# Optimization experiments

Hardware: AMD Instinct MI355X
Metric: run time of the kernel (lower is better)

The kernel has to match this reference:

```python
import jax, jax.numpy as jnp
import numpy as np

# Detect.__init__ defaults from the source
TOP_K = 5000
CONF_THRESH = 0.01
NMS_THRESH = 0.3
VAR0, VAR1 = 0.1, 0.2   # variance = [0.1, 0.2]
NUM_CLASSES = 2

B = 16
IMAGE = 1280
FMAPS = [320, 160, 80, 40, 20, 10]          # image / steps [4,8,16,32,64,128]
MIN_SIZES = [16, 32, 64, 128, 256, 512]
AR = 1.5                                     # aspect_ratios = [[1.5]] * 6


def make_priors():
    """Vectorized PriorBox.forward: 1 prior per location (max_sizes=[], single AR)."""
    chunks = []
    for f, ms in zip(FMAPS, MIN_SIZES):
        c = (np.arange(f, dtype=np.float32) + 0.5) / f
        cy, cx = np.meshgrid(c, c, indexing='ij')
        s = ms / float(IMAGE)
        w = np.full_like(cx, s / np.sqrt(AR))   # s_k / sqrt(ar)
        h = np.full_like(cx, s * np.sqrt(AR))   # s_k * sqrt(ar)
        chunks.append(np.stack([cx, cy, w, h], -1).reshape(-1, 4))
    pr = np.concatenate(chunks, 0).clip(0.0, 1.0)   # clip=True
    return jnp.asarray(pr, jnp.float32)             # [136500, 4]


def setup_inputs() -> dict:
    key = jax.random.key(0)
    k1, k2 = jax.random.split(key)
    P = sum(f * f for f in FMAPS)   # 136500
    loc_data = 0.5 * jax.random.normal(k1, (B, P, 4), jnp.float32)
    conf_data = jax.random.uniform(k2, (B * P, NUM_CLASSES), jnp.float32)  # post-softmax probs
    prior_data = make_priors()
    return {"loc_data": loc_data, "conf_data": conf_data, "prior_data": prior_data}


def _decode(loc, priors):
    # SSD box decode with variances [0.1, 0.2]; loc, priors: [P,4]
    cxcy = priors[:, :2] + loc[:, :2] * VAR0 * priors[:, 2:]
    wh = priors[:, 2:] * jnp.exp(loc[:, 2:] * VAR1)
    xy1 = cxcy - wh * 0.5
    xy2 = xy1 + wh
    return jnp.concatenate([xy1, xy2], axis=-1)   # [P,4] x1y1x2y2


def _greedy_keep(boxes, valid):
    # Greedy NMS over score-sorted candidates. boxes [K,4], valid [K] bool.
    # Indices/keep decisions are discrete -> computed on stop_gradient'd boxes.
    b = jax.lax.stop_gradient(boxes)
    x1, y1, x2, y2 = b[:, 0], b[:, 1], b[:, 2], b[:, 3]
    area = (x2 - x1) * (y2 - y1)
    idxs = jnp.arange(b.shape[0])

    def body(keep, i):
        iw = jnp.maximum(jnp.minimum(x2, x2[i]) - jnp.maximum(x1, x1[i]), 0.0)
        ih = jnp.maximum(jnp.minimum(y2, y2[i]) - jnp.maximum(y1, y1[i]), 0.0)
        inter = iw * ih
        iou = inter / (area + area[i] - inter)
        suppress = keep[i] & (iou > NMS_THRESH) & (idxs > i)
        return keep & ~suppress, None

    keep, _ = jax.lax.scan(body, valid, idxs)
    return keep


def _detect_one(loc_i, conf_cl, priors):
    # loc_i [P,4]; conf_cl [P] = class-1 scores; returns [TOP_K, 5] (score, x1,y1,x2,y2)
    boxes = _decode(loc_i, priors)
    masked = jnp.where(conf_cl > CONF_THRESH, conf_cl, -1.0)   # c_mask gating
    order = jnp.argsort(-jax.lax.stop_gradient(masked))[:TOP_K]  # scores.sort, top_k cap
    s = masked[order]
    b = boxes[order]
    valid = s > CONF_THRESH
    keep = _greedy_keep(b, valid)
    # scatter kept (score, box) rows, in descending-score order, into dense output
    rank = jnp.cumsum(keep) - 1
    row = jnp.where(keep, rank, TOP_K)            # dropped rows -> scratch slot
    vals = jnp.concatenate([s[:, None], b], axis=1)
    vals = jnp.where(keep[:, None], vals, 0.0)
    out = jnp.zeros((TOP_K + 1, 5), jnp.float32).at[row].set(vals)
    return out[:TOP_K]


def reference(loc_data, conf_data, prior_data):
    num = loc_data.shape[0]
    P = prior_data.shape[0]
    conf_preds = conf_data.reshape(num, P, NUM_CLASSES).transpose(0, 2, 1)  # [B,2,P]
    cls1 = jax.vmap(_detect_one, in_axes=(0, 0, None))(loc_data, conf_preds[:, 1, :], prior_data)
    bg = jnp.zeros_like(cls1)                     # background class row stays zero
    output = jnp.stack([bg, cls1], axis=1)        # [B, 2, TOP_K, 5]
    # NOTE: the original's final `flt[(rank < top_k)...].fill_(0)` fills a boolean-indexed
    # COPY in torch, so it is a no-op on `output`; we faithfully return output unchanged.
    return output
```

## Files before the change

kernel.cpp:

```cpp
#include <hip/hip_runtime.h>
#include <math.h>

#pragma clang fp contract(off)

#define PNUM 136500
#define HPNUM 68250
#define BNUM 16
#define TOPK 5000
#define CAP 8192
#define NB2 1024
#define B2BASE 0xBC00u
#define NWORDS 79
#define NW32 158
#define GSTRIDE 32
#define CAPE 65536
#define ELDS 10240
#define NXB 128
#define NWC 8
#define NXB2 1024
#define BSTRIDE 5120
#define EBUF 3072
#define SLOTS 4

#define OFF_SC    ((size_t)0)
#define OFF_BOX4  (OFF_SC + 320000)
#define OFF_HIST  (OFF_BOX4 + 1280000)
#define OFF_GBCUR (OFF_HIST + 65536)
#define OFF_ECNT  (OFF_GBCUR + 1048576)
#define OFF_BCNT  (OFF_ECNT + 2048)
#define OFF_BCUR  (OFF_BCNT + 65536)
#define OFF_ZEND  (OFF_BCUR + 65536)
#define OFF_CUT   (OFF_ZEND)
#define OFF_SBASE (OFF_CUT + 64)
#define OFF_KEYS  (OFF_SBASE + 65536)
#define OFF_EDGE  (OFF_KEYS + 1048576)
#define OFF_GRP   (OFF_EDGE + 4194304)
#define OFF_BOFS  (OFF_GRP)
#define OFF_SIDX  (OFF_GRP + 16384)
#define OFF_SBOX  (OFF_SIDX + 327680)

__device__ __forceinline__ unsigned f2ord(float f) {
    unsigned u = __float_as_uint(f);
    return (u & 0x80000000u) ? ~u : (u | 0x80000000u);
}
__device__ __forceinline__ float ord2f(unsigned o) {
    unsigned u = (o & 0x80000000u) ? (o ^ 0x80000000u) : ~o;
    return __uint_as_float(u);
}
__device__ __forceinline__ int bucketOf(float x) {
    int b = (int)((x + 0.6f) * 71.111115f);
    return (b < 0) ? 0 : ((b > 127) ? 127 : b);
}
__device__ __forceinline__ int rkeyOf(float x1, float x2) {
    int b = bucketOf(x1);
    int wc = bucketOf(x2) - b;
    if (wc > NWC - 1) wc = NWC - 1;
    if (wc < 0) wc = 0;
    return b * NWC + wc;
}

__global__ void __launch_bounds__(512) k_hist(const float* __restrict__ conf,
                                              unsigned* __restrict__ hist) {
    __shared__ unsigned lh[NB2];
    int img = blockIdx.y;
    for (int i = threadIdx.x; i < NB2; i += 512) lh[i] = 0;
    __syncthreads();
    const float4* src = (const float4*)(conf + (size_t)img * PNUM * 2);
    int stride = gridDim.x * 512;
    for (int q = blockIdx.x * 512 + threadIdx.x; q < HPNUM; q += stride) {
        float4 v = src[q];
        if (v.y > 0.01f) atomicAdd(&lh[(f2ord(v.y) >> 16) - B2BASE], 1u);
        if (v.w > 0.01f) atomicAdd(&lh[(f2ord(v.w) >> 16) - B2BASE], 1u);
    }
    __syncthreads();
    unsigned* h = hist + (size_t)img * NB2;
    for (int i = threadIdx.x; i < NB2; i += 512) {
        unsigned c = lh[i];
        if (c) atomicAdd(&h[i], c);
    }
}

__global__ void __launch_bounds__(256) k_cutoff2(const unsigned* __restrict__ hist,
                                                 unsigned* __restrict__ cut,
                                                 unsigned* __restrict__ sbase) {
    __shared__ unsigned csum[256], suf[256];
    int img = blockIdx.x;
    int t = threadIdx.x;
    const unsigned* h = hist + (size_t)img * NB2;
    unsigned h0 = h[t * 4], h1 = h[t * 4 + 1], h2 = h[t * 4 + 2], h3 = h[t * 4 + 3];
    csum[t] = h0 + h1 + h2 + h3;
    __syncthreads();
    if (t == 0) {
        unsigned a = 0;
        for (int g = 255; g >= 0; --g) { unsigned c = csum[g]; suf[g] = a; a += c; }
        unsigned acc = 0, before = 0;
        int c = -1;
        for (int cc = 255; cc >= 0; --cc) {
            if (acc + csum[cc] >= (unsigned)TOPK) { c = cc; before = acc; break; }
            acc += csum[cc];
        }
        unsigned cutb = B2BASE;
        if (c >= 0) {
            unsigned s2 = before;
            cutb = B2BASE + (unsigned)c * 4u;
            for (int b = c * 4 + 3; b >= c * 4; --b) {
                s2 += h[b];
                if (s2 >= (unsigned)TOPK) { cutb = B2BASE + (unsigned)b; break; }
            }
        }
        cut[img] = cutb;
    }
    __syncthreads();
    unsigned a = suf[t];
    unsigned* sb = sbase + (size_t)img * NB2 + t * 4;
    sb[3] = a;
    sb[2] = a + h3;
    sb[1] = a + h3 + h2;
    sb[0] = a + h3 + h2 + h1;
}

__global__ void __launch_bounds__(256) k_gather2(
        const float* __restrict__ conf, const unsigned* __restrict__ cut,
        const unsigned* __restrict__ sbase, unsigned* __restrict__ gbcur,
        unsigned long long* __restrict__ keys) {
    int q = blockIdx.x * 256 + threadIdx.x;
    int img = blockIdx.y;
    if (q >= HPNUM) return;
    unsigned cutb = cut[img];
    float4 v = ((const float4*)(conf + (size_t)img * PNUM * 2))[q];
    const unsigned* sb = sbase + (size_t)img * NB2;
    unsigned* gc = gbcur + (size_t)img * NB2 * 16;
    unsigned long long* kp = keys + (size_t)img * CAP;
    #pragma unroll
    for (int e = 0; e < 2; ++e) {
        float s = e ? v.w : v.y;
        if (s > 0.01f) {
            unsigned o = f2ord(s);
            if ((o >> 16) >= cutb) {
                unsigned wb = (o >> 16) - B2BASE;
                unsigned pos = sb[wb] + atomicAdd(&gc[wb * 16], 1u);
                if (pos < (unsigned)CAP)
                    kp[pos] = ((unsigned long long)o << 32)
                              | (unsigned)(~(unsigned)(2 * q + e));
            }
        }
    }
}

__global__ void __launch_bounds__(256) k_ssortdec(
        const unsigned long long* __restrict__ keys,
        const unsigned* __restrict__ hist, const unsigned* __restrict__ cut,
        const unsigned* __restrict__ sbase,
        const float* __restrict__ loc, const float* __restrict__ pri,
        float* __restrict__ SC, float4* __restrict__ BOX4,
        unsigned* __restrict__ bcnt) {
    __shared__ unsigned long long sk[1024];
    __shared__ unsigned lhist[NXB2];
    int img = blockIdx.y;
    int b = blockIdx.x;
    if (B2BASE + (unsigned)b < cut[img]) return;
    unsigned cnt = hist[(size_t)img * NB2 + b];
    if (cnt == 0) return;
    unsigned base = sbase[(size_t)img * NB2 + b];
    if (base >= (unsigned)TOPK) return;
    const unsigned long long* kp = keys + (size_t)img * CAP + base;
    int tid = threadIdx.x;
    for (int i = tid; i < NXB2; i += 256) lhist[i] = 0;
    unsigned scnt = cnt > 1024 ? 1024u : cnt;
    if (scnt >= 2) {
        unsigned np2 = 2;
        while (np2 < scnt) np2 <<= 1;
        for (unsigned i = tid; i < np2; i += 256) sk[i] = (i < scnt) ? kp[i] : 0ull;
        __syncthreads();
        for (unsigned k = 2; k <= np2; k <<= 1) {
            for (unsigned j = k >> 1; j > 0; j >>= 1) {
                for (unsigned t = tid; t < (np2 >> 1); t += 256) {
                    unsigned i = ((t & ~(j - 1)) << 1) | (t & (j - 1));
                    unsigned p = i | j;
                    bool desc = ((i & k) == 0);
                    unsigned long long a = sk[i], bb = sk[p];
                    bool sw = desc ? (a < bb) : (a > bb);
                    if (sw) { sk[i] = bb; sk[p] = a; }
                }
                __syncthreads();
            }
        }
    } else {
        if (tid == 0 && scnt == 1) sk[0] = kp[0];
        __syncthreads();
    }
    size_t ibase = (size_t)img * TOPK;
    for (unsigned i = tid; i < cnt; i += 256) {
        unsigned r = base + i;
        if (r >= (unsigned)TOPK) continue;
        unsigned long long key = (i < scnt) ? sk[i] : kp[i];
        float s, x1, y1, x2, y2;
        if (key != 0ull) {
            unsigned ordv = (unsigned)(key >> 32);
            s = ord2f(ordv);
            unsigned p = ~(unsigned)(key & 0xFFFFFFFFull);
            const float* lp = loc + ((size_t)img * PNUM + p) * 4;
            const float* pp = pri + (size_t)p * 4;
            float lx = lp[0], ly = lp[1], lw = lp[2], lh = lp[3];
            float px = pp[0], py = pp[1], pw = pp[2], ph = pp[3];
            float cx = px + (lx * 0.1f) * pw;
            float cy = py + (ly * 0.1f) * ph;
            float w = pw * expf(lw * 0.2f);
            float h = ph * expf(lh * 0.2f);
            x1 = cx - w * 0.5f;
            y1 = cy - h * 0.5f;
            x2 = x1 + w;
            y2 = y1 + h;
        } else {
            s = -1.0f; x1 = 0.f; y1 = 0.f; x2 = 0.f; y2 = 0.f;
        }
        SC[ibase + r] = s;
        BOX4[ibase + r] = make_float4(x1, y1, x2, y2);
        atomicAdd(&lhist[rkeyOf(x1, x2)], 1u);
    }
    __syncthreads();
    for (int i = tid; i < NXB2; i += 256) {
        unsigned c = lhist[i];
        if (c) atomicAdd(&bcnt[img * NXB2 + i], c);
    }
}

__global__ void __launch_bounds__(256) k_bscat(
        const unsigned* __restrict__ bcnt, unsigned* __restrict__ bcur,
        const float4* __restrict__ BOX4,
        unsigned* __restrict__ bofs, unsigned* __restrict__ sidx,
        float4* __restrict__ sbox) {
    __shared__ unsigned bpre[NXB2 + 1], tsum[256];
    int img = blockIdx.y;
    int tid = threadIdx.x;
    const unsigned* bc = bcnt + img * NXB2;
    unsigned l0 = bc[tid * 4], l1 = bc[tid * 4 + 1],
             l2 = bc[tid * 4 + 2], l3 = bc[tid * 4 + 3];
    tsum[tid] = l0 + l1 + l2 + l3;
    __syncthreads();
    if (tid == 0) {
        unsigned a = 0;
        for (int t = 0; t < 256; ++t) { unsigned c = tsum[t]; tsum[t] = a; a += c; }
        bpre[NXB2] = a;
    }
    __syncthreads();
    unsigned a = tsum[tid];
    bpre[tid * 4] = a;
    bpre[tid * 4 + 1] = a + l0;
    bpre[tid * 4 + 2] = a + l0 + l1;
    bpre[tid * 4 + 3] = a + l0 + l1 + l2;
    __syncthreads();
    if (blockIdx.x == 0) {
        if (tid < NXB) bofs[img * 130 + tid] = bpre[tid * NWC];
        if (tid == 0) bofs[img * 130 + NXB] = bpre[NXB2];
    }
    int r = blockIdx.x * 256 + tid;
    if (r < TOPK) {
        float4 b = BOX4[(size_t)img * TOPK + r];
        int bk = rkeyOf(b.x, b.z);
        unsigned s = bpre[bk] + atomicAdd(&bcur[img * NXB2 + bk], 1u);
        int base = img * BSTRIDE;
        sidx[base + s] = (unsigned)r;
        sbox[base + s] = b;
    }
}

__global__ void __launch_bounds__(256) k_pair4(
        const unsigned* __restrict__ bofs, const unsigned* __restrict__ sidx,
        const float4* __restrict__ sbox,
        unsigned* __restrict__ ecnt, unsigned* __restrict__ edges) {
    __shared__ unsigned ebuf[EBUF];
    __shared__ unsigned ecl, ebase;
    int img = blockIdx.y;
    int wid = threadIdx.x >> 6;
    int lane = threadIdx.x & 63;
    int sb0 = (blockIdx.x * 4 + wid) * SLOTS;
    if (threadIdx.x == 0) ecl = 0;
    __syncthreads();
    unsigned* ec = ecnt + (size_t)img * GSTRIDE;
    unsigned* eg = edges + (size_t)img * CAPE;
    if (sb0 < TOPK) {
        int base = img * BSTRIDE;
        float x1k[SLOTS], x2k[SLOTS], y1k[SLOTS], y2k[SLOTS], ark[SLOTS];
        unsigned rk[SLOTS];
        bool act[SLOTS];
        #pragma unroll
        for (int k = 0; k < SLOTS; ++k) {
            act[k] = (sb0 + k) < TOPK;
            int s = act[k] ? (sb0 + k) : sb0;
            float4 bk = sbox[base + s];
            x1k[k] = bk.x; y1k[k] = bk.y; x2k[k] = bk.z; y2k[k] = bk.w;
            ark[k] = (bk.z - bk.x) * (bk.w - bk.y);
            rk[k] = sidx[base + s];
        }
        int b1 = bucketOf(x1k[0]);
        int b2m = bucketOf(x2k[0]);
        #pragma unroll
        for (int k = 1; k < SLOTS; ++k)
            if (act[k]) { int b = bucketOf(x2k[k]); if (b > b2m) b2m = b; }
        const unsigned* bo = bofs + img * 130;
        unsigned s0 = bo[b1], s1 = bo[b2m + 1];
        if (s0 < s1) {
            unsigned nit = (s1 - s0 + 63) >> 6;
            unsigned c0 = s0 + (unsigned)lane;
            if (c0 > s1 - 1) c0 = s1 - 1;
            float4 cb = sbox[base + c0];
            unsigned cr = sidx[base + c0];
            for (unsigned it = 0; it < nit; ++it) {
                float4 nb = cb; unsigned nr = cr;
                if (it + 1 < nit) {
                    unsigned cn = s0 + (it + 1) * 64 + (unsigned)lane;
                    if (cn > s1 - 1) cn = s1 - 1;
                    nb = sbox[base + cn];
                    nr = sidx[base + cn];
                }
                bool in = (s0 + it * 64 + (unsigned)lane) < s1;
                float bar = (cb.z - cb.x) * (cb.w - cb.y);
                #pragma unroll
                for (int k = 0; k < SLOTS; ++k) {
                    bool hit = false;
                    unsigned edge = 0;
                    if (in && act[k] && cb.x >= x1k[k]
                        && !(cb.x == x1k[k] && cr <= rk[k])) {
                        float dx = fminf(x2k[k], cb.z) - fmaxf(x1k[k], cb.x);
                        if (dx > 0.0f) {
                            float dy = fminf(y2k[k], cb.w) - fmaxf(y1k[k], cb.y);
                            if (dy > 0.0f) {
                                float inter = dx * dy;
                                float iou = inter / (bar + ark[k] - inter);
                                if (iou > 0.3f) {
                                    unsigned su = (rk[k] < cr) ? rk[k] : cr;
                                    unsigned vi = (rk[k] < cr) ? cr : rk[k];
                                    edge = (vi << 13) | su;
                                    hit = true;
                                }
                            }
                        }
                    }
                    unsigned long long bal = __ballot(hit);
                    if (bal) {
                        int n = __popcll(bal);
                        unsigned wb = 0;
                        if (lane == 0) wb = atomicAdd(&ecl, (unsigned)n);
                        wb = __shfl(wb, 0, 64);
                        if (hit) {
                            unsigned long long lt =
                                (lane == 0) ? 0ull : ((1ull << lane) - 1ull);
                            unsigned p = wb + (unsigned)__popcll(bal & lt);
                            if (p < (unsigned)EBUF) ebuf[p] = edge;
                            else {
                                unsigned gp = atomicAdd(ec, 1u);
                                if (gp < (unsigned)CAPE) eg[gp] = edge;
                            }
                        }
                    }
                }
                cb = nb; cr = nr;
            }
        }
    }
    __syncthreads();
    unsigned n = min(ecl, (unsigned)EBUF);
    if (threadIdx.x == 0 && n) ebase = atomicAdd(ec, n);
    __syncthreads();
    for (unsigned i = threadIdx.x; i < n; i += 256) {
        unsigned p = ebase + i;
        if (p < (unsigned)CAPE) eg[p] = ebuf[i];
    }
}

__global__ void __launch_bounds__(256) k_nms3(
        const float* __restrict__ SC, const float4* __restrict__ BOX4,
        const unsigned* __restrict__ ecnt, const unsigned* __restrict__ edges,
        float* __restrict__ out) {
    __shared__ unsigned lgrp[ELDS];
    __shared__ unsigned undL[160], keptL[160], blockL[160];
    __shared__ unsigned pfx[80];
    __shared__ int chg[2];
    int img = blockIdx.x;
    int tid = threadIdx.x;
    int l = tid & 63;
    int wid = tid >> 6;
    size_t ib = (size_t)img * TOPK;
    const float* sc = SC + ib;

    float* oimg = out + (size_t)img * 2 * TOPK * 5;
    uint4* oz = (uint4*)oimg;
    uint4 z4 = make_uint4(0u, 0u, 0u, 0u);
    for (int i = tid; i < 12500; i += 256) oz[i] = z4;

    if (tid < 160) { keptL[tid] = 0u; blockL[tid] = 0u; }
    if (tid < 2) chg[tid] = 0;
    for (int w = wid; w < NWORDS; w += 4) {
        int row = w * 64 + l;
        bool valid = (row < TOPK) && (sc[row] > 0.01f);
        unsigned long long b = __ballot(valid);
        if (l == 0) {
            undL[2 * w]     = (unsigned)b;
            undL[2 * w + 1] = (unsigned)(b >> 32);
        }
    }
    unsigned E = min(ecnt[(size_t)img * GSTRIDE], (unsigned)CAPE);
    const unsigned* eimg = edges + (size_t)img * CAPE;
    bool inl = (E <= (unsigned)ELDS);
    if (inl) for (unsigned e = tid; e < E; e += 256) lgrp[e] = eimg[e];
    __syncthreads();

    for (int round = 0; round < 256; ++round) {
        int par = round & 1;
        for (unsigned e = tid; e < E; e += 256) {
            unsigned ed = inl ? lgrp[e] : eimg[e];
            unsigned s = ed & 8191u;
            unsigned v = ed >> 13;
            unsigned sw = s >> 5, sb = s & 31u;
            unsigned vw = v >> 5, vb = 1u << (v & 31u);
            if ((keptL[sw] >> sb) & 1u) {
                if (undL[vw] & vb) {
                    unsigned old = atomicAnd(&undL[vw], ~vb);
                    if (old & vb) chg[par] = 1;
                }
            } else if ((undL[sw] >> sb) & 1u) {
                if (!(blockL[vw] & vb)) atomicOr(&blockL[vw], vb);
            }
        }
        __syncthreads();
        if (tid < NW32) {
            unsigned nk = undL[tid] & ~blockL[tid];
            if (nk) {
                keptL[tid] |= nk;
                undL[tid] &= ~nk;
                chg[par] = 1;
            }
            blockL[tid] = 0u;
        }
        if (tid == 0) chg[par ^ 1] = 0;
        __syncthreads();
        if (!chg[par]) break;
    }

    if (tid == 0) {
        unsigned acc = 0;
        for (int w = 0; w < NWORDS; ++w) {
            pfx[w] = acc;
            acc += (unsigned)(__popc(keptL[2 * w]) + __popc(keptL[2 * w + 1]));
        }
    }
    __syncthreads();
    const float4* bx = BOX4 + ib;
    float* op = oimg + (size_t)TOPK * 5;
    for (int w = wid; w < NWORDS; w += 4) {
        unsigned long long kw =
            ((unsigned long long)keptL[2 * w + 1] << 32) | keptL[2 * w];
        if (!kw) continue;
        int row = w * 64 + l;
        if ((kw >> l) & 1ull) {
            int rank = (int)pfx[w] + (int)__popcll(kw & ((1ull << l) - 1ull));
            float4 b = bx[row];
            float* r = op + (size_t)rank * 5;
            r[0] = sc[row]; r[1] = b.x; r[2] = b.y; r[3] = b.z; r[4] = b.w;
        }
    }
}

extern "C" void kernel_launch(void* const* d_in, const int* in_sizes, int n_in,
                              void* d_out, int out_size, void* d_ws, size_t ws_size,
                              hipStream_t stream) {
    (void)in_sizes; (void)n_in; (void)ws_size; (void)out_size;
    const float* loc  = (const float*)d_in[0];
    const float* conf = (const float*)d_in[1];
    const float* pri  = (const float*)d_in[2];
    float* out = (float*)d_out;
    char* ws = (char*)d_ws;

    float* SC   = (float*)(ws + OFF_SC);
    float4* BOX4 = (float4*)(ws + OFF_BOX4);
    unsigned* hist = (unsigned*)(ws + OFF_HIST);
    unsigned* cut  = (unsigned*)(ws + OFF_CUT);
    unsigned* sbase = (unsigned*)(ws + OFF_SBASE);
    unsigned* gbcur = (unsigned*)(ws + OFF_GBCUR);
    unsigned long long* keys = (unsigned long long*)(ws + OFF_KEYS);
    unsigned* ecnt = (unsigned*)(ws + OFF_ECNT);
    unsigned* bcnt = (unsigned*)(ws + OFF_BCNT);
    unsigned* bcur = (unsigned*)(ws + OFF_BCUR);
    unsigned* edges = (unsigned*)(ws + OFF_EDGE);
    unsigned* bofs = (unsigned*)(ws + OFF_BOFS);
    unsigned* sidx = (unsigned*)(ws + OFF_SIDX);
    float4* sbox = (float4*)(ws + OFF_SBOX);

    hipMemsetAsync(ws + OFF_HIST, 0, OFF_ZEND - OFF_HIST, stream);

    dim3 gh1(16, BNUM);
    k_hist<<<gh1, 512, 0, stream>>>(conf, hist);
    k_cutoff2<<<BNUM, 256, 0, stream>>>(hist, cut, sbase);
    dim3 gh2((HPNUM + 255) / 256, BNUM);
    k_gather2<<<gh2, 256, 0, stream>>>(conf, cut, sbase, gbcur, keys);
    dim3 gs(NB2, BNUM);
    k_ssortdec<<<gs, 256, 0, stream>>>(keys, hist, cut, sbase,
                                       loc, pri, SC, BOX4, bcnt);
    dim3 gb((TOPK + 255) / 256, BNUM);
    k_bscat<<<gb, 256, 0, stream>>>(bcnt, bcur, BOX4, bofs, sidx, sbox);
    dim3 pg((TOPK + 4 * SLOTS - 1) / (4 * SLOTS), BNUM);
    k_pair4<<<pg, 256, 0, stream>>>(bofs, sidx, sbox, ecnt, edges);
    k_nms3<<<BNUM, 256, 0, stream>>>(SC, BOX4, ecnt, edges, out);
}
```

Measured before the change: 232.9 us.

## Refine score histogram to 4096 bins and sort only non-empty buckets via worklist

The score histogram moves from 1024 to 4096 finer bins (shift 14 instead of 16), so each bucket that must be bitonic-sorted holds fewer keys. The cutoff kernel now emits a compact worklist of non-empty buckets at or above the cutoff, and the sort/decode kernel runs a persistent grid of 1024 blocks that walks that list instead of launching NB2×16 blocks that mostly exit early. Shared-memory sort indices are padded to reduce bank conflicts and the gather counter stride shrinks. The tradeoffs are a global atomic per worklist entry, a larger histogram and workspace, and serial per-bucket loops inside each persistent block.

```diff
diff --git a/kernel.cpp b/kernel.cpp
--- a/kernel.cpp
+++ b/kernel.cpp
@@ -8,8 +8,9 @@
 #define BNUM 16
 #define TOPK 5000
 #define CAP 8192
-#define NB2 1024
-#define B2BASE 0xBC00u
+#define NB4 4096
+#define WBASE 0x2F000u
+#define GCS 4
 #define NWORDS 79
 #define NW32 158
 #define GSTRIDE 32
@@ -21,18 +22,21 @@
 #define BSTRIDE 5120
 #define EBUF 3072
 #define SLOTS 4
+#define SKI(i) ((i) + ((i) >> 4))
 
 #define OFF_SC    ((size_t)0)
 #define OFF_BOX4  (OFF_SC + 320000)
 #define OFF_HIST  (OFF_BOX4 + 1280000)
-#define OFF_GBCUR (OFF_HIST + 65536)
+#define OFF_GBCUR (OFF_HIST + 262144)
 #define OFF_ECNT  (OFF_GBCUR + 1048576)
 #define OFF_BCNT  (OFF_ECNT + 2048)
 #define OFF_BCUR  (OFF_BCNT + 65536)
-#define OFF_ZEND  (OFF_BCUR + 65536)
+#define OFF_WCNT  (OFF_BCUR + 65536)
+#define OFF_ZEND  (OFF_WCNT + 64)
 #define OFF_CUT   (OFF_ZEND)
 #define OFF_SBASE (OFF_CUT + 64)
-#define OFF_KEYS  (OFF_SBASE + 65536)
+#define OFF_WL    (OFF_SBASE + 262144)
+#define OFF_KEYS  (OFF_WL + 262144)
 #define OFF_EDGE  (OFF_KEYS + 1048576)
 #define OFF_GRP   (OFF_EDGE + 4194304)
 #define OFF_BOFS  (OFF_GRP)
@@ -61,20 +65,20 @@
 
 __global__ void __launch_bounds__(512) k_hist(const float* __restrict__ conf,
                                               unsigned* __restrict__ hist) {
-    __shared__ unsigned lh[NB2];
+    __shared__ unsigned lh[NB4];
     int img = blockIdx.y;
-    for (int i = threadIdx.x; i < NB2; i += 512) lh[i] = 0;
+    for (int i = threadIdx.x; i < NB4; i += 512) lh[i] = 0;
     __syncthreads();
     const float4* src = (const float4*)(conf + (size_t)img * PNUM * 2);
     int stride = gridDim.x * 512;
     for (int q = blockIdx.x * 512 + threadIdx.x; q < HPNUM; q += stride) {
         float4 v = src[q];
-        if (v.y > 0.01f) atomicAdd(&lh[(f2ord(v.y) >> 16) - B2BASE], 1u);
-        if (v.w > 0.01f) atomicAdd(&lh[(f2ord(v.w) >> 16) - B2BASE], 1u);
-    }
-    __syncthreads();
-    unsigned* h = hist + (size_t)img * NB2;
-    for (int i = threadIdx.x; i < NB2; i += 512) {
+        if (v.y > 0.01f) atomicAdd(&lh[(f2ord(v.y) >> 14) - WBASE], 1u);
+        if (v.w > 0.01f) atomicAdd(&lh[(f2ord(v.w) >> 14) - WBASE], 1u);
+    }
+    __syncthreads();
+    unsigned* h = hist + (size_t)img * NB4;
+    for (int i = threadIdx.x; i < NB4; i += 512) {
         unsigned c = lh[i];
         if (c) atomicAdd(&h[i], c);
     }
@@ -82,13 +86,18 @@
 
 __global__ void __launch_bounds__(256) k_cutoff2(const unsigned* __restrict__ hist,
                                                  unsigned* __restrict__ cut,
-                                                 unsigned* __restrict__ sbase) {
-    __shared__ unsigned csum[256], suf[256];
+                                                 unsigned* __restrict__ sbase,
+                                                 unsigned* __restrict__ wl,
+                                                 unsigned* __restrict__ wcnt) {
+    __shared__ unsigned csum[256], suf[256], scut;
     int img = blockIdx.x;
     int t = threadIdx.x;
-    const unsigned* h = hist + (size_t)img * NB2;
-    unsigned h0 = h[t * 4], h1 = h[t * 4 + 1], h2 = h[t * 4 + 2], h3 = h[t * 4 + 3];
-    csum[t] = h0 + h1 + h2 + h3;
+    const unsigned* h = hist + (size_t)img * NB4;
+    unsigned hv[16];
+    unsigned s = 0;
+    #pragma unroll
+    for (int j = 0; j < 16; ++j) { hv[j] = h[t * 16 + j]; s += hv[j]; }
+    csum[t] = s;
     __syncthreads();
     if (t == 0) {
         unsigned a = 0;
@@ -99,24 +108,33 @@
             if (acc + csum[cc] >= (unsigned)TOPK) { c = cc; before = acc; break; }
             acc += csum[cc];
         }
-        unsigned cutb = B2BASE;
+        unsigned cutb = WBASE;
         if (c >= 0) {
             unsigned s2 = before;
-            cutb = B2BASE + (unsigned)c * 4u;
-            for (int b = c * 4 + 3; b >= c * 4; --b) {
+            cutb = WBASE + (unsigned)c * 16u;
+            for (int b = c * 16 + 15; b >= c * 16; --b) {
                 s2 += h[b];
-                if (s2 >= (unsigned)TOPK) { cutb = B2BASE + (unsigned)b; break; }
-            }
-        }
+                if (s2 >= (unsigned)TOPK) { cutb = WBASE + (unsigned)b; break; }
+            }
+        }
+        scut = cutb;
         cut[img] = cutb;
     }
     __syncthreads();
-    unsigned a = suf[t];
-    unsigned* sb = sbase + (size_t)img * NB2 + t * 4;
-    sb[3] = a;
-    sb[2] = a + h3;
-    sb[1] = a + h3 + h2;
-    sb[0] = a + h3 + h2 + h1;
+    unsigned cutb = scut;
+    unsigned acc = suf[t];
+    unsigned* sb = sbase + (size_t)img * NB4 + t * 16;
+    sb[15] = acc;
+    #pragma unroll
+    for (int j = 14; j >= 0; --j) { acc += hv[j + 1]; sb[j] = acc; }
+    #pragma unroll
+    for (int j = 0; j < 16; ++j) {
+        unsigned b = (unsigned)t * 16u + (unsigned)j;
+        if (WBASE + b >= cutb && hv[j] > 0) {
+            unsigned x = atomicAdd(wcnt, 1u);
+            wl[x] = ((unsigned)img << 12) | b;
+        }
+    }
 }
 
 __global__ void __launch_bounds__(256) k_gather2(
@@ -128,17 +146,18 @@
     if (q >= HPNUM) return;
     unsigned cutb = cut[img];
     float4 v = ((const float4*)(conf + (size_t)img * PNUM * 2))[q];
-    const unsigned* sb = sbase + (size_t)img * NB2;
-    unsigned* gc = gbcur + (size_t)img * NB2 * 16;
+    const unsigned* sb = sbase + (size_t)img * NB4;
+    unsigned* gc = gbcur + (size_t)img * NB4 * GCS;
     unsigned long long* kp = keys + (size_t)img * CAP;
     #pragma unroll
     for (int e = 0; e < 2; ++e) {
         float s = e ? v.w : v.y;
         if (s > 0.01f) {
             unsigned o = f2ord(s);
-            if ((o >> 16) >= cutb) {
-                unsigned wb = (o >> 16) - B2BASE;
-                unsigned pos = sb[wb] + atomicAdd(&gc[wb * 16], 1u);
+            unsigned w18 = o >> 14;
+            if (w18 >= cutb) {
+                unsigned wb = w18 - WBASE;
+                unsigned pos = sb[wb] + atomicAdd(&gc[wb * GCS], 1u);
                 if (pos < (unsigned)CAP)
                     kp[pos] = ((unsigned long long)o << 32)
                               | (unsigned)(~(unsigned)(2 * q + e));
@@ -149,79 +168,83 @@
 
 __global__ void __launch_bounds__(256) k_ssortdec(
         const unsigned long long* __restrict__ keys,
-        const unsigned* __restrict__ hist, const unsigned* __restrict__ cut,
-        const unsigned* __restrict__ sbase,
+        const unsigned* __restrict__ hist, const unsigned* __restrict__ sbase,
+        const unsigned* __restrict__ wl, const unsigned* __restrict__ wcnt,
         const float* __restrict__ loc, const float* __restrict__ pri,
         float* __restrict__ SC, float4* __restrict__ BOX4,
         unsigned* __restrict__ bcnt) {
-    __shared__ unsigned long long sk[1024];
+    __shared__ unsigned long long sk[1088];
     __shared__ unsigned lhist[NXB2];
-    int img = blockIdx.y;
-    int b = blockIdx.x;
-    if (B2BASE + (unsigned)b < cut[img]) return;
-    unsigned cnt = hist[(size_t)img * NB2 + b];
-    if (cnt == 0) return;
-    unsigned base = sbase[(size_t)img * NB2 + b];
-    if (base >= (unsigned)TOPK) return;
-    const unsigned long long* kp = keys + (size_t)img * CAP + base;
     int tid = threadIdx.x;
-    for (int i = tid; i < NXB2; i += 256) lhist[i] = 0;
-    unsigned scnt = cnt > 1024 ? 1024u : cnt;
-    if (scnt >= 2) {
-        unsigned np2 = 2;
-        while (np2 < scnt) np2 <<= 1;
-        for (unsigned i = tid; i < np2; i += 256) sk[i] = (i < scnt) ? kp[i] : 0ull;
+    unsigned nW = *wcnt;
+    for (unsigned w = blockIdx.x; w < nW; w += gridDim.x) {
+        unsigned ent = wl[w];
+        int img = (int)(ent >> 12);
+        int b = (int)(ent & 4095u);
+        unsigned cnt = hist[(size_t)img * NB4 + b];
+        unsigned base = sbase[(size_t)img * NB4 + b];
+        if (base >= (unsigned)TOPK) continue;
+        const unsigned long long* kp = keys + (size_t)img * CAP + base;
+        for (int i = tid; i < NXB2; i += 256) lhist[i] = 0;
+        unsigned scnt = cnt > 1024 ? 1024u : cnt;
+        if (scnt >= 2) {
+            unsigned np2 = 2;
+            while (np2 < scnt) np2 <<= 1;
+            for (unsigned i = tid; i < np2; i += 256)
+                sk[SKI(i)] = (i < scnt) ? kp[i] : 0ull;
+            __syncthreads();
+            for (unsigned k = 2; k <= np2; k <<= 1) {
+                for (unsigned j = k >> 1; j > 0; j >>= 1) {
+                    for (unsigned t = tid; t < (np2 >> 1); t += 256) {
+                        unsigned i = ((t & ~(j - 1)) << 1) | (t & (j - 1));
+                        unsigned p = i | j;
+                        bool desc = ((i & k) == 0);
+                        unsigned long long a = sk[SKI(i)], bb = sk[SKI(p)];
+                        bool sw = desc ? (a < bb) : (a > bb);
+                        if (sw) { sk[SKI(i)] = bb; sk[SKI(p)] = a; }
+                    }
+                    __syncthreads();
+                }
+            }
+        } else {
+            if (tid == 0 && scnt == 1) sk[0] = kp[0];
+            __syncthreads();
+        }
+        size_t ibase = (size_t)img * TOPK;
+        for (unsigned i = tid; i < cnt; i += 256) {
+            unsigned r = base + i;
+            if (r >= (unsigned)TOPK) continue;
+            unsigned long long key = (i < scnt) ? sk[SKI(i)] : kp[i];
+            float s, x1, y1, x2, y2;
+            if (key != 0ull) {
+                unsigned ordv = (unsigned)(key >> 32);
+                s = ord2f(ordv);
+                unsigned p = ~(unsigned)(key & 0xFFFFFFFFull);
+                const float* lp = loc + ((size_t)img * PNUM + p) * 4;
+                const float* pp = pri + (size_t)p * 4;
+                float lx = lp[0], ly = lp[1], lw = lp[2], lh = lp[3];
+                float px = pp[0], py = pp[1], pw = pp[2], ph = pp[3];
+                float cx = px + (lx * 0.1f) * pw;
+                float cy = py + (ly * 0.1f) * ph;
+                float w2 = pw * expf(lw * 0.2f);
+                float h2 = ph * expf(lh * 0.2f);
+                x1 = cx - w2 * 0.5f;
+                y1 = cy - h2 * 0.5f;
+                x2 = x1 + w2;
+                y2 = y1 + h2;
+            } else {
+                s = -1.0f; x1 = 0.f; y1 = 0.f; x2 = 0.f; y2 = 0.f;
+            }
+            SC[ibase + r] = s;
+            BOX4[ibase + r] = make_float4(x1, y1, x2, y2);
+            atomicAdd(&lhist[rkeyOf(x1, x2)], 1u);
+        }
         __syncthreads();
-        for (unsigned k = 2; k <= np2; k <<= 1) {
-            for (unsigned j = k >> 1; j > 0; j >>= 1) {
-                for (unsigned t = tid; t < (np2 >> 1); t += 256) {
-                    unsigned i = ((t & ~(j - 1)) << 1) | (t & (j - 1));
-                    unsigned p = i | j;
-                    bool desc = ((i & k) == 0);
-                    unsigned long long a = sk[i], bb = sk[p];
-                    bool sw = desc ? (a < bb) : (a > bb);
-                    if (sw) { sk[i] = bb; sk[p] = a; }
-                }
-                __syncthreads();
-            }
-        }
-    } else {
-        if (tid == 0 && scnt == 1) sk[0] = kp[0];
+        for (int i = tid; i < NXB2; i += 256) {
+            unsigned c = lhist[i];
+            if (c) atomicAdd(&bcnt[img * NXB2 + i], c);
+        }
         __syncthreads();
-    }
-    size_t ibase = (size_t)img * TOPK;
-    for (unsigned i = tid; i < cnt; i += 256) {
-        unsigned r = base + i;
-        if (r >= (unsigned)TOPK) continue;
-        unsigned long long key = (i < scnt) ? sk[i] : kp[i];
-        float s, x1, y1, x2, y2;
-        if (key != 0ull) {
-            unsigned ordv = (unsigned)(key >> 32);
-            s = ord2f(ordv);
-            unsigned p = ~(unsigned)(key & 0xFFFFFFFFull);
-            const float* lp = loc + ((size_t)img * PNUM + p) * 4;
-            const float* pp = pri + (size_t)p * 4;
-            float lx = lp[0], ly = lp[1], lw = lp[2], lh = lp[3];
-            float px = pp[0], py = pp[1], pw = pp[2], ph = pp[3];
-            float cx = px + (lx * 0.1f) * pw;
-            float cy = py + (ly * 0.1f) * ph;
-            float w = pw * expf(lw * 0.2f);
-            float h = ph * expf(lh * 0.2f);
-            x1 = cx - w * 0.5f;
-            y1 = cy - h * 0.5f;
-            x2 = x1 + w;
-            y2 = y1 + h;
-        } else {
-            s = -1.0f; x1 = 0.f; y1 = 0.f; x2 = 0.f; y2 = 0.f;
-        }
-        SC[ibase + r] = s;
-        BOX4[ibase + r] = make_float4(x1, y1, x2, y2);
-        atomicAdd(&lhist[rkeyOf(x1, x2)], 1u);
-    }
-    __syncthreads();
-    for (int i = tid; i < NXB2; i += 256) {
-        unsigned c = lhist[i];
-        if (c) atomicAdd(&bcnt[img * NXB2 + i], c);
     }
 }
 
@@ -482,6 +505,8 @@
     unsigned* ecnt = (unsigned*)(ws + OFF_ECNT);
     unsigned* bcnt = (unsigned*)(ws + OFF_BCNT);
     unsigned* bcur = (unsigned*)(ws + OFF_BCUR);
+    unsigned* wcnt = (unsigned*)(ws + OFF_WCNT);
+    unsigned* wl   = (unsigned*)(ws + OFF_WL);
     unsigned* edges = (unsigned*)(ws + OFF_EDGE);
     unsigned* bofs = (unsigned*)(ws + OFF_BOFS);
     unsigned* sidx = (unsigned*)(ws + OFF_SIDX);
@@ -491,12 +516,11 @@
 
     dim3 gh1(16, BNUM);
     k_hist<<<gh1, 512, 0, stream>>>(conf, hist);
-    k_cutoff2<<<BNUM, 256, 0, stream>>>(hist, cut, sbase);
+    k_cutoff2<<<BNUM, 256, 0, stream>>>(hist, cut, sbase, wl, wcnt);
     dim3 gh2((HPNUM + 255) / 256, BNUM);
     k_gather2<<<gh2, 256, 0, stream>>>(conf, cut, sbase, gbcur, keys);
-    dim3 gs(NB2, BNUM);
-    k_ssortdec<<<gs, 256, 0, stream>>>(keys, hist, cut, sbase,
-                                       loc, pri, SC, BOX4, bcnt);
+    k_ssortdec<<<1024, 256, 0, stream>>>(keys, hist, sbase, wl, wcnt,
+                                         loc, pri, SC, BOX4, bcnt);
     dim3 gb((TOPK + 255) / 256, BNUM);
     k_bscat<<<gb, 256, 0, stream>>>(bcnt, bcur, BOX4, bofs, sidx, sbox);
     dim3 pg((TOPK + 4 * SLOTS - 1) / (4 * SLOTS), BNUM);
```

Result: faster. 212.6 us (-8.7%).
